# Kernel optimization log

Measured on AMD Instinct MI355X. Metric: run time of the kernel, lower is better.

The kernel has to match this reference:

```python
import jax, jax.numpy as jnp
import numpy as np

N_QUBITS = 4
N_LAYERS = 2
DIM = 2 ** N_QUBITS  # 16
B = 262144


def _cnot_perm(c, t):
    # wire 0 is the most significant bit (pennylane default.qubit convention)
    idx = np.arange(DIM)
    cb = (idx >> (N_QUBITS - 1 - c)) & 1
    return idx ^ (cb << (N_QUBITS - 1 - t))

# all-pairs CNOTs (i, j) for i < j, applied once per layer
CNOT_PERMS = [jnp.asarray(_cnot_perm(i, j)) for i in range(N_QUBITS) for j in range(i + 1, N_QUBITS)]


def _rx(t):
    c = jnp.cos(t / 2).astype(jnp.complex64)
    s = jnp.sin(t / 2).astype(jnp.complex64)
    return jnp.stack([jnp.stack([c, -1j * s], -1), jnp.stack([-1j * s, c], -1)], -2)


def _ry(t):
    c = jnp.cos(t / 2).astype(jnp.complex64)
    s = jnp.sin(t / 2).astype(jnp.complex64)
    return jnp.stack([jnp.stack([c, -s], -1), jnp.stack([s, c], -1)], -2)


def _rz(t):
    e = jnp.exp(-1j * t.astype(jnp.complex64) / 2)
    z = jnp.zeros_like(e)
    return jnp.stack([jnp.stack([e, z], -1), jnp.stack([z, jnp.conj(e)], -1)], -2)


def _apply_1q(state, gate, wire):
    # state: [B, 2,2,2,2]; gate: [2,2] (shared) or [B,2,2] (per-sample)
    ax = 1 + wire
    s = jnp.moveaxis(state, ax, -1)
    if gate.ndim == 2:
        s = jnp.einsum('b...i,ji->b...j', s, gate)
    else:
        s = jnp.einsum('b...i,bji->b...j', s, gate)
    return jnp.moveaxis(s, -1, ax)


def _circuit(x, qw):
    # x: [B, 4] rotation angles; qw: [24] circuit weights. Returns <Z_0>: [B]
    b = x.shape[0]
    state = jnp.zeros((b, DIM), jnp.complex64).at[:, 0].set(1.0)
    state = state.reshape((b,) + (2,) * N_QUBITS)
    for i in range(N_QUBITS):
        state = _apply_1q(state, _rx(x[:, i]), i)
        state = _apply_1q(state, _rz(x[:, i]), i)
    for layer in range(N_LAYERS):
        for i in range(N_QUBITS):
            state = _apply_1q(state, _ry(qw[layer * N_QUBITS + i]), i)
            state = _apply_1q(state, _rz(qw[layer * N_QUBITS + i + N_QUBITS]), i)
        flat = state.reshape(b, DIM)
        for p in CNOT_PERMS:
            flat = flat[:, p]
        state = flat.reshape((b,) + (2,) * N_QUBITS)
        for i in range(N_QUBITS):
            state = _apply_1q(state, _rx(qw[layer * N_QUBITS + i + 2 * N_QUBITS]), i)
    probs = jnp.abs(state.reshape(b, DIM)) ** 2
    zvec = jnp.where(jnp.arange(DIM) < DIM // 2, 1.0, -1.0).astype(probs.dtype)
    return probs @ zvec


def _mlp(q, W1, b1, W2, b2, W3, b3, W4, b4):
    h = jax.nn.relu(q @ W1.T + b1)
    h = jax.nn.relu(h @ W2.T + b2)
    h = jax.nn.relu(h @ W3.T + b3)
    return jax.nn.sigmoid(h @ W4.T + b4)


def setup_inputs() -> dict:
    key = jax.random.key(0)
    ks = jax.random.split(key, 10)
    def lin(k, fo, fi):
        bound = 1.0 / np.sqrt(fi)
        k1, k2 = jax.random.split(k)
        return (jax.random.uniform(k1, (fo, fi), jnp.float32, -bound, bound),
                jax.random.uniform(k2, (fo,), jnp.float32, -bound, bound))
    W1, b1 = lin(ks[2], 32, 1)
    W2, b2 = lin(ks[3], 16, 32)
    W3, b3 = lin(ks[4], 8, 16)
    W4, b4 = lin(ks[5], 1, 8)
    return {
        'x': jax.random.normal(ks[0], (B, N_QUBITS), jnp.float32),
        'qw': jax.random.normal(ks[1], (N_LAYERS * N_QUBITS * 3,), jnp.float32),
        'W1': W1, 'b1': b1, 'W2': W2, 'b2': b2,
        'W3': W3, 'b3': b3, 'W4': W4, 'b4': b4,
    }


def reference(x, qw, W1, b1, W2, b2, W3, b3, W4, b4):
    q = _circuit(x, qw)[:, None]  # [B, 1] quantum expectation values
    return _mlp(q, W1, b1, W2, b2, W3, b3, W4, b4)
```

## Files before the change

### kernel.cpp

```cpp
#include <hip/hip_runtime.h>
#include <math.h>

#define DIM 16
#define LUT_N 4096

__global__ void qnn_setup(const float* __restrict__ qw,
                          const float* __restrict__ W1, const float* __restrict__ b1,
                          const float* __restrict__ W2, const float* __restrict__ b2,
                          const float* __restrict__ W3, const float* __restrict__ b3,
                          const float* __restrict__ W4, const float* __restrict__ b4,
                          float* __restrict__ ws) {
  int gid = blockIdx.x * blockDim.x + threadIdx.x;

  if (gid <= LUT_N) {
    float q = (float)(gid - LUT_N / 2) * (2.0f / LUT_N);
    float h1[32];
#pragma unroll
    for (int j = 0; j < 32; ++j) h1[j] = fmaxf(0.f, fmaf(q, W1[j], b1[j]));
    float h2[16];
#pragma unroll
    for (int k = 0; k < 16; ++k) {
      float acc = b2[k];
#pragma unroll
      for (int j = 0; j < 32; ++j) acc = fmaf(W2[k * 32 + j], h1[j], acc);
      h2[k] = fmaxf(0.f, acc);
    }
    float h3[8];
#pragma unroll
    for (int k = 0; k < 8; ++k) {
      float acc = b3[k];
#pragma unroll
      for (int j = 0; j < 16; ++j) acc = fmaf(W3[k * 16 + j], h2[j], acc);
      h3[k] = fmaxf(0.f, acc);
    }
    float acc = b4[0];
#pragma unroll
    for (int j = 0; j < 8; ++j) acc = fmaf(W4[j], h3[j], acc);
    ws[64 + gid] = 1.f / (1.f + expf(-acc));
  } else if (gid >= 4104 && gid < 4108) {
    int w = gid - 4104;
    float a  = qw[0 + w];
    float b  = qw[4 + w];
    float e0 = qw[8 + w];
    float c  = qw[4 + w];
    float d  = qw[8 + w];
    float e1 = qw[12 + w];

    ws[w * 4 + 0] = cosf(0.5f * a);
    ws[w * 4 + 1] = sinf(0.5f * a);
    ws[w * 4 + 2] = cosf(0.5f * b);
    ws[w * 4 + 3] = sinf(0.5f * b);

    float cc = cosf(0.5f * c), sc = sinf(0.5f * c);
    float ce = cosf(0.5f * e0), se = sinf(0.5f * e0);
    float m00r = cc * ce,  m00i =  sc * se;
    float m01r = -sc * ce, m01i = -cc * se;
    float m10r =  sc * ce, m10i = -cc * se;
    float m11r =  cc * ce, m11i = -sc * se;
    float cd = cosf(0.5f * d), sd = sinf(0.5f * d);
    float* u = ws + 16 + w * 8;
    u[0] = cd * m00r + sd * m00i;  u[1] = cd * m00i - sd * m00r;
    u[2] = cd * m01r + sd * m01i;  u[3] = cd * m01i - sd * m01r;
    u[4] = cd * m10r - sd * m10i;  u[5] = cd * m10i + sd * m10r;
    u[6] = cd * m11r - sd * m11i;  u[7] = cd * m11i + sd * m11r;

    if (w == 0) {
      ws[48] = cosf(e1);
      ws[49] = sinf(e1);
    }
  }
}

__device__ __forceinline__ void cmul(float ar, float ai, float br, float bi,
                                     float& cr, float& ci) {
  cr = ar * br - ai * bi;
  ci = ar * bi + ai * br;
}

template <int TB>
__device__ __forceinline__ void apply_u(float (&sr)[DIM], float (&si)[DIM],
                                        float u00r, float u00i, float u01r, float u01i,
                                        float u10r, float u10i, float u11r, float u11i) {
#pragma unroll
  for (int i = 0; i < DIM; ++i) {
    if (i & TB) continue;
    const int j = i | TB;
    float ar = sr[i], ai = si[i], br = sr[j], bi = si[j];
    float nr = u00r * ar - u00i * ai + u01r * br - u01i * bi;
    float ni = u00r * ai + u00i * ar + u01r * bi + u01i * br;
    float mr = u10r * ar - u10i * ai + u11r * br - u11i * bi;
    float mi = u10r * ai + u10i * ar + u11r * bi + u11i * br;
    sr[i] = nr; si[i] = ni; sr[j] = mr; si[j] = mi;
  }
}

template <int CB, int TB>
__device__ __forceinline__ void apply_cnot(float (&sr)[DIM], float (&si)[DIM]) {
#pragma unroll
  for (int i = 0; i < DIM; ++i) {
    if (!(i & CB)) continue;
    if (i & TB) continue;
    const int j = i | TB;
    float tr = sr[i], ti = si[i];
    sr[i] = sr[j]; si[i] = si[j];
    sr[j] = tr;    si[j] = ti;
  }
}

__global__ __launch_bounds__(256) void qnn_kernel(
    const float* __restrict__ x, const float* __restrict__ ws,
    float* __restrict__ out, int B) {
  int b = blockIdx.x * blockDim.x + threadIdx.x;
  if (b >= B) return;

  float4 xv = reinterpret_cast<const float4*>(x)[b];
  float xs[4] = {xv.x, xv.y, xv.z, xv.w};

  float ur[4][2], ui[4][2];
#pragma unroll
  for (int w = 0; w < 4; ++w) {
    float s, c;
    __sincosf(0.5f * xs[w], &s, &c);
    float v0r0 = c * c, v0i0 = -c * s;
    float v0r1 = s * s, v0i1 = -c * s;
    float cy = ws[w * 4 + 0], sy = ws[w * 4 + 1];
    float cz = ws[w * 4 + 2], sz = ws[w * 4 + 3];
    float t0r = cy * v0r0 - sy * v0r1, t0i = cy * v0i0 - sy * v0i1;
    float t1r = sy * v0r0 + cy * v0r1, t1i = sy * v0i0 + cy * v0i1;
    ur[w][0] = cz * t0r + sz * t0i;  ui[w][0] = cz * t0i - sz * t0r;
    ur[w][1] = cz * t1r - sz * t1i;  ui[w][1] = cz * t1i + sz * t1r;
  }

  float a01r[4], a01i[4], a23r[4], a23i[4];
#pragma unroll
  for (int i0 = 0; i0 < 2; ++i0)
#pragma unroll
    for (int i1 = 0; i1 < 2; ++i1) {
      cmul(ur[0][i0], ui[0][i0], ur[1][i1], ui[1][i1], a01r[i0 * 2 + i1], a01i[i0 * 2 + i1]);
      cmul(ur[2][i0], ui[2][i0], ur[3][i1], ui[3][i1], a23r[i0 * 2 + i1], a23i[i0 * 2 + i1]);
    }
  float sr[DIM], si[DIM];
#pragma unroll
  for (int i = 0; i < DIM; ++i)
    cmul(a01r[i >> 2], a01i[i >> 2], a23r[i & 3], a23i[i & 3], sr[i], si[i]);

  apply_cnot<8, 4>(sr, si);
  apply_cnot<8, 2>(sr, si);
  apply_cnot<8, 1>(sr, si);
  apply_cnot<4, 2>(sr, si);
  apply_cnot<4, 1>(sr, si);
  apply_cnot<2, 1>(sr, si);

#define APPLY_U(WIRE, TB)                                                   \
  apply_u<TB>(sr, si, ws[16 + WIRE * 8 + 0], ws[16 + WIRE * 8 + 1],         \
              ws[16 + WIRE * 8 + 2], ws[16 + WIRE * 8 + 3],                 \
              ws[16 + WIRE * 8 + 4], ws[16 + WIRE * 8 + 5],                 \
              ws[16 + WIRE * 8 + 6], ws[16 + WIRE * 8 + 7]);
  APPLY_U(0, 8)
  APPLY_U(1, 4)
  APPLY_U(2, 2)
  APPLY_U(3, 1)
#undef APPLY_U

  apply_cnot<8, 4>(sr, si);
  apply_cnot<8, 2>(sr, si);
  apply_cnot<8, 1>(sr, si);
  apply_cnot<4, 2>(sr, si);
  apply_cnot<4, 1>(sr, si);
  apply_cnot<2, 1>(sr, si);

  float ez = 0.f, ey = 0.f;
#pragma unroll
  for (int i = 0; i < 8; ++i) {
    const int j = i + 8;
    ez += sr[i] * sr[i] + si[i] * si[i] - sr[j] * sr[j] - si[j] * si[j];
    ey += sr[i] * si[j] - si[i] * sr[j];
  }
  float q = ws[48] * ez + ws[49] * (2.f * ey);

  const float* lut = ws + 64;
  float t = fmaf(q, (float)(LUT_N / 2), (float)(LUT_N / 2));
  t = fminf(fmaxf(t, 0.f), (float)LUT_N);
  int i0 = min((int)t, LUT_N - 1);
  float frac = t - (float)i0;
  float f0 = lut[i0], f1 = lut[i0 + 1];
  out[b] = fmaf(frac, f1 - f0, f0);
}

extern "C" void kernel_launch(void* const* d_in, const int* in_sizes, int n_in,
                              void* d_out, int out_size, void* d_ws, size_t ws_size,
                              hipStream_t stream) {
  const float* x  = (const float*)d_in[0];
  const float* qw = (const float*)d_in[1];
  const float* W1 = (const float*)d_in[2];
  const float* b1 = (const float*)d_in[3];
  const float* W2 = (const float*)d_in[4];
  const float* b2 = (const float*)d_in[5];
  const float* W3 = (const float*)d_in[6];
  const float* b3 = (const float*)d_in[7];
  const float* W4 = (const float*)d_in[8];
  const float* b4 = (const float*)d_in[9];
  float* out = (float*)d_out;
  float* ws  = (float*)d_ws;

  qnn_setup<<<17, 256, 0, stream>>>(qw, W1, b1, W2, b2, W3, b3, W4, b4, ws);

  const int B = in_sizes[0] / 4;
  const int block = 256;
  const int grid = (B + block - 1) / block;
  qnn_kernel<<<grid, block, 0, stream>>>(x, ws, out, B);
}
```

Before: 88.68 us.

## Precompute Pauli-basis coefficient tensor so per-sample expectation is a polynomial contraction

The setup kernel now builds the full 16x16 circuit unitary in shared memory, forms the Heisenberg-picture observable U†ZU, and expands it into a 256-entry Pauli-product coefficient tensor. The main kernel then evaluates each sample's expectation as a 4x4x4x4 contraction over per-wire trigonometric features (1, sin², -sin·cos, cos), with no per-sample state-vector simulation. This cuts per-thread arithmetic and register use. The cost is 256 broadcast coefficient loads per thread and a serialised single-block setup with many __syncthreads.

Result: slower. 96.99 us (+9.4%).

```diff
diff --git a/kernel.cpp b/kernel.cpp
--- a/kernel.cpp
+++ b/kernel.cpp
@@ -1,8 +1,63 @@
 #include <hip/hip_runtime.h>
 #include <math.h>
 
-#define DIM 16
 #define LUT_N 4096
+
+
+__device__ __forceinline__ float mlp_eval(float q,
+                                          const float* __restrict__ W1, const float* __restrict__ b1,
+                                          const float* __restrict__ W2, const float* __restrict__ b2,
+                                          const float* __restrict__ W3, const float* __restrict__ b3,
+                                          const float* __restrict__ W4, const float* __restrict__ b4) {
+  float h1[32];
+#pragma unroll
+  for (int j = 0; j < 32; ++j) h1[j] = fmaxf(0.f, fmaf(q, W1[j], b1[j]));
+  float h2[16];
+#pragma unroll
+  for (int k = 0; k < 16; ++k) {
+    float acc = b2[k];
+#pragma unroll
+    for (int j = 0; j < 32; ++j) acc = fmaf(W2[k * 32 + j], h1[j], acc);
+    h2[k] = fmaxf(0.f, acc);
+  }
+  float h3[8];
+#pragma unroll
+  for (int k = 0; k < 8; ++k) {
+    float acc = b3[k];
+#pragma unroll
+    for (int j = 0; j < 16; ++j) acc = fmaf(W3[k * 16 + j], h2[j], acc);
+    h3[k] = fmaxf(0.f, acc);
+  }
+  float acc = b4[0];
+#pragma unroll
+  for (int j = 0; j < 8; ++j) acc = fmaf(W4[j], h3[j], acc);
+  return 1.f / (1.f + expf(-acc));
+}
+
+__device__ __forceinline__ void g1q(float (*Ur)[16], float (*Ui)[16], int r, int c, int w,
+                                    float u00r, float u00i, float u01r, float u01i,
+                                    float u10r, float u10i, float u11r, float u11i) {
+  const int tb = 8 >> w;
+  const int bit = (r & tb) ? 1 : 0;
+  const int rp = r ^ tb;
+  float ar = Ur[r][c], ai = Ui[r][c];
+  float br = Ur[rp][c], bi = Ui[rp][c];
+  __syncthreads();
+  float dr = bit ? u11r : u00r, di = bit ? u11i : u00i;
+  float fr = bit ? u10r : u01r, fi = bit ? u10i : u01i;
+  Ur[r][c] = dr * ar - di * ai + fr * br - fi * bi;
+  Ui[r][c] = dr * ai + di * ar + fr * bi + fi * br;
+  __syncthreads();
+}
+
+__device__ __forceinline__ void gcnot(float (*Ur)[16], float (*Ui)[16], int r, int c,
+                                      int cc, int tt) {
+  int src = r ^ ((((r >> (3 - cc)) & 1)) << (3 - tt));
+  float ar = Ur[src][c], ai = Ui[src][c];
+  __syncthreads();
+  Ur[r][c] = ar; Ui[r][c] = ai;
+  __syncthreads();
+}
 
 __global__ void qnn_setup(const float* __restrict__ qw,
                           const float* __restrict__ W1, const float* __restrict__ b1,
@@ -10,101 +65,88 @@
                           const float* __restrict__ W3, const float* __restrict__ b3,
                           const float* __restrict__ W4, const float* __restrict__ b4,
                           float* __restrict__ ws) {
-  int gid = blockIdx.x * blockDim.x + threadIdx.x;
-
-  if (gid <= LUT_N) {
+  if (blockIdx.x < 16) {
+    int gid = blockIdx.x * 256 + threadIdx.x;
     float q = (float)(gid - LUT_N / 2) * (2.0f / LUT_N);
-    float h1[32];
-#pragma unroll
-    for (int j = 0; j < 32; ++j) h1[j] = fmaxf(0.f, fmaf(q, W1[j], b1[j]));
-    float h2[16];
-#pragma unroll
-    for (int k = 0; k < 16; ++k) {
-      float acc = b2[k];
-#pragma unroll
-      for (int j = 0; j < 32; ++j) acc = fmaf(W2[k * 32 + j], h1[j], acc);
-      h2[k] = fmaxf(0.f, acc);
-    }
-    float h3[8];
-#pragma unroll
-    for (int k = 0; k < 8; ++k) {
-      float acc = b3[k];
-#pragma unroll
-      for (int j = 0; j < 16; ++j) acc = fmaf(W3[k * 16 + j], h2[j], acc);
-      h3[k] = fmaxf(0.f, acc);
-    }
-    float acc = b4[0];
-#pragma unroll
-    for (int j = 0; j < 8; ++j) acc = fmaf(W4[j], h3[j], acc);
-    ws[64 + gid] = 1.f / (1.f + expf(-acc));
-  } else if (gid >= 4104 && gid < 4108) {
-    int w = gid - 4104;
-    float a  = qw[0 + w];
-    float b  = qw[4 + w];
-    float e0 = qw[8 + w];
-    float c  = qw[4 + w];
-    float d  = qw[8 + w];
-    float e1 = qw[12 + w];
-
-    ws[w * 4 + 0] = cosf(0.5f * a);
-    ws[w * 4 + 1] = sinf(0.5f * a);
-    ws[w * 4 + 2] = cosf(0.5f * b);
-    ws[w * 4 + 3] = sinf(0.5f * b);
-
-    float cc = cosf(0.5f * c), sc = sinf(0.5f * c);
-    float ce = cosf(0.5f * e0), se = sinf(0.5f * e0);
-    float m00r = cc * ce,  m00i =  sc * se;
-    float m01r = -sc * ce, m01i = -cc * se;
-    float m10r =  sc * ce, m10i = -cc * se;
-    float m11r =  cc * ce, m11i = -sc * se;
-    float cd = cosf(0.5f * d), sd = sinf(0.5f * d);
-    float* u = ws + 16 + w * 8;
-    u[0] = cd * m00r + sd * m00i;  u[1] = cd * m00i - sd * m00r;
-    u[2] = cd * m01r + sd * m01i;  u[3] = cd * m01i - sd * m01r;
-    u[4] = cd * m10r - sd * m10i;  u[5] = cd * m10i + sd * m10r;
-    u[6] = cd * m11r - sd * m11i;  u[7] = cd * m11i + sd * m11r;
-
-    if (w == 0) {
-      ws[48] = cosf(e1);
-      ws[49] = sinf(e1);
-    }
-  }
-}
-
-__device__ __forceinline__ void cmul(float ar, float ai, float br, float bi,
-                                     float& cr, float& ci) {
-  cr = ar * br - ai * bi;
-  ci = ar * bi + ai * br;
-}
-
-template <int TB>
-__device__ __forceinline__ void apply_u(float (&sr)[DIM], float (&si)[DIM],
-                                        float u00r, float u00i, float u01r, float u01i,
-                                        float u10r, float u10i, float u11r, float u11i) {
-#pragma unroll
-  for (int i = 0; i < DIM; ++i) {
-    if (i & TB) continue;
-    const int j = i | TB;
-    float ar = sr[i], ai = si[i], br = sr[j], bi = si[j];
-    float nr = u00r * ar - u00i * ai + u01r * br - u01i * bi;
-    float ni = u00r * ai + u00i * ar + u01r * bi + u01i * br;
-    float mr = u10r * ar - u10i * ai + u11r * br - u11i * bi;
-    float mi = u10r * ai + u10i * ar + u11r * bi + u11i * br;
-    sr[i] = nr; si[i] = ni; sr[j] = mr; si[j] = mi;
-  }
-}
-
-template <int CB, int TB>
-__device__ __forceinline__ void apply_cnot(float (&sr)[DIM], float (&si)[DIM]) {
-#pragma unroll
-  for (int i = 0; i < DIM; ++i) {
-    if (!(i & CB)) continue;
-    if (i & TB) continue;
-    const int j = i | TB;
-    float tr = sr[i], ti = si[i];
-    sr[i] = sr[j]; si[i] = si[j];
-    sr[j] = tr;    si[j] = ti;
-  }
+    ws[256 + gid] = mlp_eval(q, W1, b1, W2, b2, W3, b3, W4, b4);
+    return;
+  }
+
+  __shared__ float Ur[16][16], Ui[16][16], Opr[16][16], Opi[16][16];
+  const int t = threadIdx.x;
+  const int r = t >> 4, c = t & 15;
+
+  Ur[r][c] = (r == c) ? 1.f : 0.f;
+  Ui[r][c] = 0.f;
+  __syncthreads();
+
+#pragma unroll
+  for (int l = 0; l < 2; ++l) {
+#pragma unroll
+    for (int w = 0; w < 4; ++w) {
+      float ty = qw[l * 4 + w];
+      float sy = sinf(0.5f * ty), cy = cosf(0.5f * ty);
+      g1q(Ur, Ui, r, c, w, cy, 0.f, -sy, 0.f, sy, 0.f, cy, 0.f);
+      float tz = qw[l * 4 + w + 4];
+      float sz = sinf(0.5f * tz), cz = cosf(0.5f * tz);
+      g1q(Ur, Ui, r, c, w, cz, -sz, 0.f, 0.f, 0.f, 0.f, cz, sz);
+    }
+    gcnot(Ur, Ui, r, c, 0, 1);
+    gcnot(Ur, Ui, r, c, 0, 2);
+    gcnot(Ur, Ui, r, c, 0, 3);
+    gcnot(Ur, Ui, r, c, 1, 2);
+    gcnot(Ur, Ui, r, c, 1, 3);
+    gcnot(Ur, Ui, r, c, 2, 3);
+#pragma unroll
+    for (int w = 0; w < 4; ++w) {
+      float tx = qw[l * 4 + w + 8];
+      float sx = sinf(0.5f * tx), cx = cosf(0.5f * tx);
+      g1q(Ur, Ui, r, c, w, cx, 0.f, 0.f, -sx, 0.f, -sx, cx, 0.f);
+    }
+  }
+
+  float opr = 0.f, opi = 0.f;
+#pragma unroll
+  for (int k = 0; k < 16; ++k) {
+    float zk = (k < 8) ? 1.f : -1.f;
+    float ar = Ur[k][r], ai = -Ui[k][r];
+    float br = Ur[k][c], bi = Ui[k][c];
+    opr += zk * (ar * br - ai * bi);
+    opi += zk * (ar * bi + ai * br);
+  }
+  __syncthreads();
+  Opr[r][c] = opr;
+  Opi[r][c] = opi;
+  __syncthreads();
+
+  const int p0 = (t >> 6) & 3, p1 = (t >> 4) & 3, p2 = (t >> 2) & 3, p3 = t & 3;
+  const int pw[4] = {p0, p1, p2, p3};
+  float sr = 0.f;
+#pragma unroll
+  for (int j = 0; j < 16; ++j) {
+    int i = j;
+    float cr = 1.f, ci = 0.f;
+#pragma unroll
+    for (int w = 0; w < 4; ++w) {
+      int jb = (j >> (3 - w)) & 1;
+      int p = pw[w];
+      if (p == 1) {
+        i ^= 8 >> w;
+      } else if (p == 2) {
+        i ^= 8 >> w;
+        float f = jb ? 1.f : -1.f;
+        float nr = -ci * f, ni = cr * f;
+        cr = nr; ci = ni;
+      } else if (p == 3) {
+        float f = jb ? -1.f : 1.f;
+        cr *= f; ci *= f;
+      }
+    }
+    sr += Opr[i][j] * cr - Opi[i][j] * ci;
+  }
+  ws[t] = sr * (1.f / 16.f);
+
+  if (t == 0) ws[256 + LUT_N] = mlp_eval(1.f, W1, b1, W2, b2, W3, b3, W4, b4);
 }
 
 __global__ __launch_bounds__(256) void qnn_kernel(
@@ -116,73 +158,42 @@
   float4 xv = reinterpret_cast<const float4*>(x)[b];
   float xs[4] = {xv.x, xv.y, xv.z, xv.w};
 
-  float ur[4][2], ui[4][2];
+  float E[4][4];
 #pragma unroll
   for (int w = 0; w < 4; ++w) {
     float s, c;
-    __sincosf(0.5f * xs[w], &s, &c);
-    float v0r0 = c * c, v0i0 = -c * s;
-    float v0r1 = s * s, v0i1 = -c * s;
-    float cy = ws[w * 4 + 0], sy = ws[w * 4 + 1];
-    float cz = ws[w * 4 + 2], sz = ws[w * 4 + 3];
-    float t0r = cy * v0r0 - sy * v0r1, t0i = cy * v0i0 - sy * v0i1;
-    float t1r = sy * v0r0 + cy * v0r1, t1i = sy * v0i0 + cy * v0i1;
-    ur[w][0] = cz * t0r + sz * t0i;  ui[w][0] = cz * t0i - sz * t0r;
-    ur[w][1] = cz * t1r - sz * t1i;  ui[w][1] = cz * t1i + sz * t1r;
-  }
-
-  float a01r[4], a01i[4], a23r[4], a23i[4];
-#pragma unroll
-  for (int i0 = 0; i0 < 2; ++i0)
-#pragma unroll
-    for (int i1 = 0; i1 < 2; ++i1) {
-      cmul(ur[0][i0], ui[0][i0], ur[1][i1], ui[1][i1], a01r[i0 * 2 + i1], a01i[i0 * 2 + i1]);
-      cmul(ur[2][i0], ui[2][i0], ur[3][i1], ui[3][i1], a23r[i0 * 2 + i1], a23i[i0 * 2 + i1]);
-    }
-  float sr[DIM], si[DIM];
-#pragma unroll
-  for (int i = 0; i < DIM; ++i)
-    cmul(a01r[i >> 2], a01i[i >> 2], a23r[i & 3], a23i[i & 3], sr[i], si[i]);
-
-  apply_cnot<8, 4>(sr, si);
-  apply_cnot<8, 2>(sr, si);
-  apply_cnot<8, 1>(sr, si);
-  apply_cnot<4, 2>(sr, si);
-  apply_cnot<4, 1>(sr, si);
-  apply_cnot<2, 1>(sr, si);
-
-#define APPLY_U(WIRE, TB)                                                   \
-  apply_u<TB>(sr, si, ws[16 + WIRE * 8 + 0], ws[16 + WIRE * 8 + 1],         \
-              ws[16 + WIRE * 8 + 2], ws[16 + WIRE * 8 + 3],                 \
-              ws[16 + WIRE * 8 + 4], ws[16 + WIRE * 8 + 5],                 \
-              ws[16 + WIRE * 8 + 6], ws[16 + WIRE * 8 + 7]);
-  APPLY_U(0, 8)
-  APPLY_U(1, 4)
-  APPLY_U(2, 2)
-  APPLY_U(3, 1)
-#undef APPLY_U
-
-  apply_cnot<8, 4>(sr, si);
-  apply_cnot<8, 2>(sr, si);
-  apply_cnot<8, 1>(sr, si);
-  apply_cnot<4, 2>(sr, si);
-  apply_cnot<4, 1>(sr, si);
-  apply_cnot<2, 1>(sr, si);
-
-  float ez = 0.f, ey = 0.f;
-#pragma unroll
-  for (int i = 0; i < 8; ++i) {
-    const int j = i + 8;
-    ez += sr[i] * sr[i] + si[i] * si[i] - sr[j] * sr[j] - si[j] * si[j];
-    ey += sr[i] * si[j] - si[i] * sr[j];
-  }
-  float q = ws[48] * ez + ws[49] * (2.f * ey);
-
-  const float* lut = ws + 64;
-  float t = fmaf(q, (float)(LUT_N / 2), (float)(LUT_N / 2));
-  t = fminf(fmaxf(t, 0.f), (float)LUT_N);
-  int i0 = min((int)t, LUT_N - 1);
-  float frac = t - (float)i0;
+    __sincosf(xs[w], &s, &c);
+    E[w][0] = 1.f;
+    E[w][1] = s * s;
+    E[w][2] = -s * c;
+    E[w][3] = c;
+  }
+
+  float q = 0.f;
+#pragma unroll
+  for (int a = 0; a < 4; ++a) {
+    float ta = 0.f;
+#pragma unroll
+    for (int bb = 0; bb < 4; ++bb) {
+      float tb = 0.f;
+#pragma unroll
+      for (int cc = 0; cc < 4; ++cc) {
+        const float* kp = ws + (((a * 4 + bb) * 4 + cc) * 4);
+        float tc = fmaf(kp[3], E[3][3],
+                   fmaf(kp[2], E[3][2],
+                   fmaf(kp[1], E[3][1], kp[0])));
+        tb = fmaf(tc, E[2][cc], tb);
+      }
+      ta = fmaf(tb, E[1][bb], ta);
+    }
+    q = fmaf(ta, E[0][a], q);
+  }
+
+  const float* lut = ws + 256;
+  float tt = fmaf(q, (float)(LUT_N / 2), (float)(LUT_N / 2));
+  tt = fminf(fmaxf(tt, 0.f), (float)LUT_N);
+  int i0 = min((int)tt, LUT_N - 1);
+  float frac = tt - (float)i0;
   float f0 = lut[i0], f1 = lut[i0 + 1];
   out[b] = fmaf(frac, f1 - f0, f0);
 }
```
